# Kernel tuning notes

Measured on AMD Instinct MI355X. Metric: run time of the kernel, lower is better.

Reference implementation:

```python
import jax, jax.numpy as jnp
import numpy as np

WS = 2   # window_size
NH = 8   # num_heads


def window_attn(x, Wqkv, bqkv, scale, ws=WS, nh=NH):
    # x: (B, H, W, C) -> tiny ws*ws-token windowed MHA, faithful to torch reshape order
    B, H, W, C = x.shape
    hg, wg = H // ws, W // ws
    hd = C // nh
    xw = x.reshape(B, hg, ws, wg, ws, C).transpose(0, 1, 3, 2, 4, 5)  # (B,hg,wg,ws,ws,C)
    qkv = (xw @ Wqkv + bqkv).reshape(B, hg * wg, ws * ws, 3, nh, hd)
    q, k, v = jnp.transpose(qkv, (3, 0, 1, 4, 2, 5))  # each (B,G,nh,n,hd), n=ws*ws
    attn = jax.nn.softmax(jnp.einsum('bgnqd,bgnkd->bgnqk', q, k) * scale, axis=-1)
    o = jnp.einsum('bgnqk,bgnkd->bgnqd', attn, v)
    o = o.transpose(0, 1, 3, 2, 4).reshape(B, hg, wg, ws, ws, C)
    return o.transpose(0, 1, 3, 2, 4, 5).reshape(B, H, W, C)


def reference(x, Wqkv, bqkv, Wproj, bproj):
    B, C, H, W = x.shape
    scale = (C // NH) ** (-0.5)
    xr = x.reshape(B, H, W, C)  # raw reshape (NOT a transpose) -- faithful to source

    # --- Global path ---
    g = window_attn(xr, Wqkv, bqkv, scale) @ Wproj + bproj

    # --- Local path ---
    l = xr.reshape(B, C, H, W)                         # raw reshape, as in source
    l = l.reshape(B, C, H // 2, 2, W // 2, 2).mean(axis=(3, 5))  # AvgPool2d(2)
    h, w = H // 2, W // 2
    l = l.reshape(B, h, w, C)                          # raw reshape, as in source
    l = window_attn(l, Wqkv, bqkv, scale)
    l = l.reshape(B, C, h, w)                          # raw reshape, as in source
    # attn_x: reflect-pad top by 1, AvgPool2d((2,1), stride=1)
    px = jnp.pad(l, ((0, 0), (0, 0), (1, 0), (0, 0)), mode='reflect')
    lx = 0.5 * (px[:, :, :-1, :] + px[:, :, 1:, :])
    # attn_y: reflect-pad right by 1, AvgPool2d((1,2), stride=1)
    py = jnp.pad(l, ((0, 0), (0, 0), (0, 0), (0, 1)), mode='reflect')
    ly = 0.5 * (py[..., :-1] + py[..., 1:])
    # bilinear upsample x2, align_corners=False (half-pixel, matches jax.image.resize)
    l = jax.image.resize(lx + ly, (B, C, H, W), method='bilinear')
    l = l.reshape(B, H, W, C)                          # raw reshape, as in source

    return (g + l).transpose(0, 3, 1, 2)  # (B, C, H, W)


def setup_inputs() -> dict:
    key = jax.random.key(0)
    k1, k2, k3, k4, k5 = jax.random.split(key, 5)
    B, C, H, W = 4, 512, 128, 128
    x = jax.random.normal(k1, (B, C, H, W), dtype=jnp.float32)
    Wqkv = jax.random.normal(k2, (C, 3 * C), dtype=jnp.float32) * 0.02
    bqkv = jax.random.normal(k3, (3 * C,), dtype=jnp.float32) * 0.02
    Wproj = jax.random.normal(k4, (C, C), dtype=jnp.float32) * 0.02
    bproj = jax.random.normal(k5, (C,), dtype=jnp.float32) * 0.02
    return {'x': x, 'Wqkv': Wqkv, 'bqkv': bqkv, 'Wproj': Wproj, 'bproj': bproj}
```

## Files before the change

### kernel.cpp

```cpp
#include <hip/hip_runtime.h>

typedef float f32x4 __attribute__((ext_vector_type(4)));
typedef float f32x2 __attribute__((ext_vector_type(2)));
typedef __bf16 bf16x8 __attribute__((ext_vector_type(8)));
typedef __bf16 bf16x4 __attribute__((ext_vector_type(4)));

__device__ __forceinline__ void gll16(const void* g, void* l) {
  __builtin_amdgcn_global_load_lds(
      (const __attribute__((address_space(1))) uint32_t*)g,
      (__attribute__((address_space(3))) uint32_t*)l, 16, 0, 0);
}

__global__ __launch_bounds__(512, 2) void gemm256(
    const __bf16* __restrict__ A, const __bf16* __restrict__ BT,
    const float* __restrict__ bias, __bf16* __restrict__ C, int N, int gx)
{
  __shared__ __bf16 As[2][16384];
  __shared__ __bf16 Bs[2][16384];
  const int tid = threadIdx.x;
  const int wave = tid >> 6, lane = tid & 63;
  const int wr = (wave >> 2) * 128;
  const int wc = (wave & 3) * 64;
  const int l15 = lane & 15, l4 = lane >> 4;

  int lin = blockIdx.x;
  int olin = (lin & 7) * ((int)gridDim.x >> 3) + (lin >> 3);
  int bn = olin % gx, bm = olin / gx;
  const long arow0 = (long)bm * 256;
  const long brow0 = (long)bn * 256;

  const int srow = tid >> 3;
  const int sgc = ((tid & 7) ^ (srow & 7)) * 8;

  f32x4 acc[8][4] = {};

  auto stage = [&](int p, int kt) {
    #pragma unroll
    for (int s = 0; s < 4; s++) {
      int row = srow + s * 64;
      gll16(A  + (arow0 + row) * 512 + kt + sgc, (char*)As[p] + s * 8192 + tid * 16);
      gll16(BT + (brow0 + row) * 512 + kt + sgc, (char*)Bs[p] + s * 8192 + tid * 16);
    }
  };

  stage(0, 0);
  __syncthreads();

  for (int t = 0; t < 8; t++) {
    int cur = t & 1;
    if (t < 7) stage(cur ^ 1, (t + 1) * 64);
    #pragma unroll
    for (int kk = 0; kk < 2; kk++) {
      bf16x8 af[8], bfr[4];
      #pragma unroll
      for (int m = 0; m < 8; m++) {
        int row = wr + m * 16 + l15;
        int cp = ((kk * 4 + l4) ^ (row & 7)) * 8;
        af[m] = *(const bf16x8*)&As[cur][row * 64 + cp];
      }
      #pragma unroll
      for (int n = 0; n < 4; n++) {
        int row = wc + n * 16 + l15;
        int cp = ((kk * 4 + l4) ^ (row & 7)) * 8;
        bfr[n] = *(const bf16x8*)&Bs[cur][row * 64 + cp];
      }
      #pragma unroll
      for (int m = 0; m < 8; m++)
        #pragma unroll
        for (int n = 0; n < 4; n++)
          acc[m][n] = __builtin_amdgcn_mfma_f32_16x16x32_bf16(bfr[n], af[m], acc[m][n], 0, 0, 0);
    }
    if (t < 7) __syncthreads();
  }

  #pragma unroll
  for (int m = 0; m < 8; m++) {
    long row = arow0 + wr + m * 16 + l15;
    __bf16* crow = C + row * (long)N + brow0;
    #pragma unroll
    for (int n = 0; n < 4; n++) {
      f32x4 bv = *(const f32x4*)(bias + brow0 + wc + n * 16 + l4 * 4);
      bf16x4 o;
      #pragma unroll
      for (int k = 0; k < 4; k++) o[k] = (__bf16)(acc[m][n][k] + bv[k]);
      *(bf16x4*)(crow + wc + n * 16 + l4 * 4) = o;
    }
  }
}

__global__ __launch_bounds__(256) void attn4(
    const __bf16* __restrict__ qkv, __bf16* __restrict__ o,
    int nwin, int wg, int Wimg, int wpb, int bst)
{
  int tid = blockIdx.x * 256 + threadIdx.x;
  int m = tid & 3;
  int head = (tid >> 2) & 7;
  int win = tid >> 5;
  if (win >= nwin) return;
  int b = win / wpb, wrm = win % wpb;
  int i = wrm / wg, j = wrm % wg;
  int t0 = b * bst + 2 * i * Wimg + 2 * j;
  int tn[4] = { t0, t0 + 1, t0 + Wimg, t0 + Wimg + 1 };
  int trow = tn[m];
  const int co = head * 64;

  float qf[64];
  #pragma unroll
  for (int c = 0; c < 8; c++) {
    bf16x8 v = *(const bf16x8*)(qkv + (long)trow * 1536 + co + c * 8);
    #pragma unroll
    for (int e = 0; e < 8; e++) qf[c * 8 + e] = (float)v[e];
  }

  float s[4];
  #pragma unroll
  for (int n = 0; n < 4; n++) {
    float acc = 0.f;
    #pragma unroll
    for (int c = 0; c < 8; c++) {
      bf16x8 kv = *(const bf16x8*)(qkv + (long)tn[n] * 1536 + 512 + co + c * 8);
      #pragma unroll
      for (int e = 0; e < 8; e++) acc += qf[c * 8 + e] * (float)kv[e];
    }
    s[n] = acc * 0.125f;
  }

  float mx = fmaxf(fmaxf(s[0], s[1]), fmaxf(s[2], s[3]));
  float e0 = __expf(s[0] - mx), e1 = __expf(s[1] - mx),
        e2 = __expf(s[2] - mx), e3 = __expf(s[3] - mx);
  float inv = 1.f / (e0 + e1 + e2 + e3);
  float w4[4] = { e0 * inv, e1 * inv, e2 * inv, e3 * inv };

  float of[64] = {};
  #pragma unroll
  for (int n = 0; n < 4; n++) {
    float wn = w4[n];
    #pragma unroll
    for (int c = 0; c < 8; c++) {
      bf16x8 vv = *(const bf16x8*)(qkv + (long)tn[n] * 1536 + 1024 + co + c * 8);
      #pragma unroll
      for (int e = 0; e < 8; e++) of[c * 8 + e] += wn * (float)vv[e];
    }
  }

  #pragma unroll
  for (int c = 0; c < 8; c++) {
    bf16x8 ov;
    #pragma unroll
    for (int e = 0; e < 8; e++) ov[e] = (__bf16)of[c * 8 + e];
    *(bf16x8*)(o + (long)trow * 512 + co + c * 8) = ov;
  }
}

__global__ __launch_bounds__(256) void transpose_f32_bf16(
    const float* __restrict__ in, __bf16* __restrict__ out, int K, int N)
{
  __shared__ float t[64][65];
  int n0 = blockIdx.x * 64, k0 = blockIdx.y * 64;
  int tid = threadIdx.x;
  int nl4 = (tid & 15) * 4, kl = tid >> 4;
  #pragma unroll
  for (int p = 0; p < 4; p++) {
    int kk = kl + p * 16;
    f32x4 v = *(const f32x4*)(in + (long)(k0 + kk) * N + n0 + nl4);
    t[kk][nl4 + 0] = v.x; t[kk][nl4 + 1] = v.y; t[kk][nl4 + 2] = v.z; t[kk][nl4 + 3] = v.w;
  }
  __syncthreads();
  int ks = tid & 63, wv = tid >> 6;
  #pragma unroll
  for (int p = 0; p < 16; p++) {
    int nn = wv * 16 + p;
    out[(long)(n0 + nn) * K + k0 + ks] = (__bf16)t[ks][nn];
  }
}

__global__ __launch_bounds__(256) void convpool(const float* __restrict__ x,
    __bf16* __restrict__ Xbf, __bf16* __restrict__ P)
{
  int t = blockIdx.x * 256 + threadIdx.x;
  int j8 = (t & 15) * 8;
  int i2 = (t >> 4) & 63;
  long bc = t >> 10;
  const float* r0 = x + bc * 16384 + (2 * i2) * 128 + j8;
  f32x4 a0 = *(const f32x4*)r0,         a1 = *(const f32x4*)(r0 + 4);
  f32x4 b0 = *(const f32x4*)(r0 + 128), b1 = *(const f32x4*)(r0 + 132);
  bf16x8 xa, xb;
  xa[0] = (__bf16)a0.x; xa[1] = (__bf16)a0.y; xa[2] = (__bf16)a0.z; xa[3] = (__bf16)a0.w;
  xa[4] = (__bf16)a1.x; xa[5] = (__bf16)a1.y; xa[6] = (__bf16)a1.z; xa[7] = (__bf16)a1.w;
  xb[0] = (__bf16)b0.x; xb[1] = (__bf16)b0.y; xb[2] = (__bf16)b0.z; xb[3] = (__bf16)b0.w;
  xb[4] = (__bf16)b1.x; xb[5] = (__bf16)b1.y; xb[6] = (__bf16)b1.z; xb[7] = (__bf16)b1.w;
  *(bf16x8*)(Xbf + bc * 16384 + (2 * i2) * 128 + j8) = xa;
  *(bf16x8*)(Xbf + bc * 16384 + (2 * i2) * 128 + 128 + j8) = xb;
  bf16x4 p;
  p[0] = (__bf16)((a0.x + a0.y + b0.x + b0.y) * 0.25f);
  p[1] = (__bf16)((a0.z + a0.w + b0.z + b0.w) * 0.25f);
  p[2] = (__bf16)((a1.x + a1.y + b1.x + b1.y) * 0.25f);
  p[3] = (__bf16)((a1.z + a1.w + b1.z + b1.w) * 0.25f);
  *(bf16x4*)(P + bc * 4096 + i2 * 64 + (t & 15) * 4) = p;
}

__global__ __launch_bounds__(256) void final_v4(
    const __bf16* __restrict__ G, const __bf16* __restrict__ Ol, float* __restrict__ out)
{
  __shared__ float smem[12352];
  float (*t)[65] = (float(*)[65])smem;
  float* Sl = smem + 4160;
  __bf16* lbuf = (__bf16*)smem;

  int b = blockIdx.z;
  int p0 = blockIdx.y * 64, c0 = blockIdx.x * 64;
  int tid = threadIdx.x;

  {
    const __bf16* src = Ol + ((long)b * 512 + (long)blockIdx.y * 2) * 4096;
    #pragma unroll
    for (int i = 0; i < 4; i++)
      *(bf16x8*)&lbuf[i * 2048 + tid * 8] = *(const bf16x8*)(src + i * 2048 + tid * 8);
  }
  __syncthreads();

  #pragma unroll
  for (int k = 0; k < 32; k++) {
    int s = tid + k * 256;
    int j = s & 63, i = (s >> 6) & 63, lc = s >> 12;
    const __bf16* base = lbuf + lc * 4096;
    int im1 = (i == 0) ? 1 : i - 1;
    int jp1 = (j == 63) ? 62 : j + 1;
    Sl[s] = 0.5f * (float)base[im1 * 64 + j] + (float)base[i * 64 + j]
          + 0.5f * (float)base[i * 64 + jp1];
  }
  __syncthreads();

  int cl4 = (tid & 15) * 4, pl = tid >> 4;
  const __bf16* Gb = G + ((long)b * 16384 + p0) * 512 + c0;
  #pragma unroll
  for (int q2 = 0; q2 < 4; q2++) {
    int pp = pl + q2 * 16;
    bf16x4 g = *(const bf16x4*)(Gb + (long)pp * 512 + cl4);
    int q = (p0 + pp) * 512 + c0 + cl4;
    int lc = (q >> 14) & 1;
    int r = q & 16383, hh = r >> 7, ww0 = r & 127;
    const float* sb = Sl + lc * 4096;
    int i0, i1; float wi0, wi1;
    if (hh & 1) { i0 = hh >> 1; i1 = (i0 < 63) ? i0 + 1 : 63; wi0 = 0.75f; wi1 = 0.25f; }
    else        { i1 = hh >> 1; i0 = (i1 > 0) ? i1 - 1 : 0;   wi0 = 0.25f; wi1 = 0.75f; }
    int k = ww0 >> 1;
    int cm1 = (k > 0) ? k - 1 : 0;
    int cp2 = (k < 62) ? k + 2 : 63;
    const float* r0p = sb + i0 * 64;
    const float* r1p = sb + i1 * 64;
    float a0 = r0p[cm1], a1 = r0p[k], a2 = r0p[k + 1], a3 = r0p[cp2];
    float b0 = r1p[cm1], b1 = r1p[k], b2 = r1p[k + 1], b3 = r1p[cp2];
    float h0 = wi0 * (0.25f * a0 + 0.75f * a1) + wi1 * (0.25f * b0 + 0.75f * b1);
    float h1 = wi0 * (0.75f * a1 + 0.25f * a2) + wi1 * (0.75f * b1 + 0.25f * b2);
    float h2 = wi0 * (0.25f * a1 + 0.75f * a2) + wi1 * (0.25f * b1 + 0.75f * b2);
    float h3 = wi0 * (0.75f * a2 + 0.25f * a3) + wi1 * (0.75f * b2 + 0.25f * b3);
    t[pp][cl4 + 0] = (float)g[0] + h0;
    t[pp][cl4 + 1] = (float)g[1] + h1;
    t[pp][cl4 + 2] = (float)g[2] + h2;
    t[pp][cl4 + 3] = (float)g[3] + h3;
  }
  __syncthreads();
  int l15b = tid & 15, hi = (tid >> 4) & 3, wv = tid >> 6;
  float* ob = out + (long)b * 8388608 + (long)c0 * 16384 + p0;
  #pragma unroll
  for (int it = 0; it < 4; it++) {
    int cc = wv * 16 + it * 4 + hi;
    f32x4 v;
    v.x = t[l15b * 4 + 0][cc]; v.y = t[l15b * 4 + 1][cc];
    v.z = t[l15b * 4 + 2][cc]; v.w = t[l15b * 4 + 3][cc];
    *(f32x4*)(ob + (long)cc * 16384 + l15b * 4) = v;
  }
}

extern "C" void kernel_launch(void* const* d_in, const int* in_sizes, int n_in,
                              void* d_out, int out_size, void* d_ws, size_t ws_size,
                              hipStream_t stream)
{
  const float* x     = (const float*)d_in[0];
  const float* Wqkv  = (const float*)d_in[1];
  const float* bqkv  = (const float*)d_in[2];
  const float* Wproj = (const float*)d_in[3];
  const float* bproj = (const float*)d_in[4];
  float* out = (float*)d_out;

  char* w = (char*)d_ws;
  __bf16* WqkvT  = (__bf16*)w;  w += (size_t)1536 * 512 * 2;
  __bf16* WprojT = (__bf16*)w;  w += (size_t)512 * 512 * 2;
  __bf16* Xbf    = (__bf16*)w;  w += (size_t)65536 * 512 * 2;
  __bf16* G      = Xbf;
  __bf16* P      = (__bf16*)w;  w += (size_t)2048 * 4096 * 2;

  bool batched = ws_size >= ((size_t)356 << 20);
  size_t mchunk = batched ? 65536 : 16384;
  __bf16* QKVbuf = (__bf16*)w;  w += mchunk * 1536 * 2;
  __bf16* Obuf   = (__bf16*)w;

  transpose_f32_bf16<<<dim3(24, 8), 256, 0, stream>>>(Wqkv, WqkvT, 512, 1536);
  transpose_f32_bf16<<<dim3(8, 8), 256, 0, stream>>>(Wproj, WprojT, 512, 512);
  convpool<<<8192, 256, 0, stream>>>(x, Xbf, P);

  int nch = batched ? 1 : 4;
  int mrows = (int)mchunk;
  for (int c = 0; c < nch; c++) {
    const __bf16* Ac = Xbf + (size_t)c * 16384 * 512;
    gemm256<<<(mrows / 256) * 6, 512, 0, stream>>>(Ac, WqkvT, bqkv, QKVbuf, 1536, 6);
    attn4<<<(mrows / 4) * 32 / 256, 256, 0, stream>>>(
        QKVbuf, Obuf, mrows / 4, 64, 128, 4096, 16384);
    gemm256<<<(mrows / 256) * 2, 512, 0, stream>>>(
        Obuf, WprojT, bproj, G + (size_t)c * 16384 * 512, 512, 2);
  }

  gemm256<<<(16384 / 256) * 6, 512, 0, stream>>>(P, WqkvT, bqkv, QKVbuf, 1536, 6);
  attn4<<<512, 256, 0, stream>>>(QKVbuf, Obuf, 4096, 32, 64, 1024, 4096);

  final_v4<<<dim3(8, 256, 4), 256, 0, stream>>>(G, Obuf, out);
}
```

Before: 452.0 us.

## Split GEMM main loop into four phases interleaving chunked loads with MFMA

The GEMM k-loop is restructured into four sub-phases per k-tile. Each phase issues one quarter of the next tile's global-to-LDS loads, then computes one quadrant of the output tile, with explicit barriers, vmcnt waits and raised wave priority around the MFMAs. The goal is to spread load issue across the compute and hide memory latency better than staging the whole tile at once. The final epilogue kernel also remaps block indices so consecutive blocks touch different row regions, which may improve cache or channel locality. The extra barriers per tile add sync overhead, and the hand-written vmcnt counts must match the loads actually in flight.

```diff
diff --git a/kernel.cpp b/kernel.cpp
--- a/kernel.cpp
+++ b/kernel.cpp
@@ -11,7 +11,7 @@
       (__attribute__((address_space(3))) uint32_t*)l, 16, 0, 0);
 }
 
-__global__ __launch_bounds__(512, 2) void gemm256(
+__global__ __launch_bounds__(512, 2) void gemm256_8ph(
     const __bf16* __restrict__ A, const __bf16* __restrict__ BT,
     const float* __restrict__ bias, __bf16* __restrict__ C, int N, int gx)
 {
@@ -34,43 +34,65 @@
 
   f32x4 acc[8][4] = {};
 
-  auto stage = [&](int p, int kt) {
-    #pragma unroll
-    for (int s = 0; s < 4; s++) {
-      int row = srow + s * 64;
-      gll16(A  + (arow0 + row) * 512 + kt + sgc, (char*)As[p] + s * 8192 + tid * 16);
-      gll16(BT + (brow0 + row) * 512 + kt + sgc, (char*)Bs[p] + s * 8192 + tid * 16);
-    }
+  auto stage_chunk = [&](int p, int kt, int q) {
+    int row = srow + q * 64;
+    gll16(A  + (arow0 + row) * 512 + kt + sgc, (char*)As[p] + q * 8192 + tid * 16);
+    gll16(BT + (brow0 + row) * 512 + kt + sgc, (char*)Bs[p] + q * 8192 + tid * 16);
   };
 
-  stage(0, 0);
-  __syncthreads();
+  #pragma unroll
+  for (int q = 0; q < 4; q++) stage_chunk(0, 0, q);
 
   for (int t = 0; t < 8; t++) {
-    int cur = t & 1;
-    if (t < 7) stage(cur ^ 1, (t + 1) * 64);
-    #pragma unroll
-    for (int kk = 0; kk < 2; kk++) {
-      bf16x8 af[8], bfr[4];
+    int cur = t & 1, nxt = cur ^ 1;
+    __builtin_amdgcn_sched_barrier(0);
+    __builtin_amdgcn_s_barrier();
+    __builtin_amdgcn_sched_barrier(0);
+    if (t < 7) {
+      stage_chunk(nxt, (t + 1) * 64, 0);
+      asm volatile("s_waitcnt vmcnt(2)" ::: "memory");
+    } else {
+      asm volatile("s_waitcnt vmcnt(0)" ::: "memory");
+    }
+    __builtin_amdgcn_sched_barrier(0);
+    __builtin_amdgcn_s_barrier();
+    __builtin_amdgcn_sched_barrier(0);
+
+    #pragma unroll
+    for (int q = 0; q < 4; q++) {
+      if (q > 0) {
+        __builtin_amdgcn_sched_barrier(0);
+        __builtin_amdgcn_s_barrier();
+        __builtin_amdgcn_sched_barrier(0);
+        if (t < 7) stage_chunk(nxt, (t + 1) * 64, q);
+      }
+      const int mh = q >> 1, nh = q & 1;
       #pragma unroll
-      for (int m = 0; m < 8; m++) {
-        int row = wr + m * 16 + l15;
-        int cp = ((kk * 4 + l4) ^ (row & 7)) * 8;
-        af[m] = *(const bf16x8*)&As[cur][row * 64 + cp];
+      for (int kk = 0; kk < 2; kk++) {
+        bf16x8 af[4], bfr[2];
+        #pragma unroll
+        for (int i = 0; i < 4; i++) {
+          int row = wr + (mh * 4 + i) * 16 + l15;
+          int cp = (((kk * 4 + l4) ^ (row & 7))) * 8;
+          af[i] = *(const bf16x8*)&As[cur][row * 64 + cp];
+        }
+        #pragma unroll
+        for (int j = 0; j < 2; j++) {
+          int row = wc + (nh * 2 + j) * 16 + l15;
+          int cp = (((kk * 4 + l4) ^ (row & 7))) * 8;
+          bfr[j] = *(const bf16x8*)&Bs[cur][row * 64 + cp];
+        }
+        __builtin_amdgcn_s_setprio(1);
+        #pragma unroll
+        for (int i = 0; i < 4; i++)
+          #pragma unroll
+          for (int j = 0; j < 2; j++)
+            acc[mh * 4 + i][nh * 2 + j] =
+                __builtin_amdgcn_mfma_f32_16x16x32_bf16(bfr[j], af[i],
+                                                        acc[mh * 4 + i][nh * 2 + j], 0, 0, 0);
+        __builtin_amdgcn_s_setprio(0);
       }
-      #pragma unroll
-      for (int n = 0; n < 4; n++) {
-        int row = wc + n * 16 + l15;
-        int cp = ((kk * 4 + l4) ^ (row & 7)) * 8;
-        bfr[n] = *(const bf16x8*)&Bs[cur][row * 64 + cp];
-      }
-      #pragma unroll
-      for (int m = 0; m < 8; m++)
-        #pragma unroll
-        for (int n = 0; n < 4; n++)
-          acc[m][n] = __builtin_amdgcn_mfma_f32_16x16x32_bf16(bfr[n], af[m], acc[m][n], 0, 0, 0);
-    }
-    if (t < 7) __syncthreads();
+    }
   }
 
   #pragma unroll
@@ -199,7 +221,7 @@
   *(bf16x4*)(P + bc * 4096 + i2 * 64 + (t & 15) * 4) = p;
 }
 
-__global__ __launch_bounds__(256) void final_v4(
+__global__ __launch_bounds__(256) void final_v5(
     const __bf16* __restrict__ G, const __bf16* __restrict__ Ol, float* __restrict__ out)
 {
   __shared__ float smem[12352];
@@ -207,12 +229,16 @@
   float* Sl = smem + 4160;
   __bf16* lbuf = (__bf16*)smem;
 
+  int lin = blockIdx.x + (blockIdx.y << 3);
+  int r = lin & 7, k = lin >> 3;
+  int yy = r * 32 + (k >> 3);
+  int xx = k & 7;
   int b = blockIdx.z;
-  int p0 = blockIdx.y * 64, c0 = blockIdx.x * 64;
+  int p0 = yy * 64, c0 = xx * 64;
   int tid = threadIdx.x;
 
   {
-    const __bf16* src = Ol + ((long)b * 512 + (long)blockIdx.y * 2) * 4096;
+    const __bf16* src = Ol + ((long)b * 512 + (long)yy * 2) * 4096;
     #pragma unroll
     for (int i = 0; i < 4; i++)
       *(bf16x8*)&lbuf[i * 2048 + tid * 8] = *(const bf16x8*)(src + i * 2048 + tid * 8);
@@ -220,8 +246,8 @@
   __syncthreads();
 
   #pragma unroll
-  for (int k = 0; k < 32; k++) {
-    int s = tid + k * 256;
+  for (int kq = 0; kq < 32; kq++) {
+    int s = tid + kq * 256;
     int j = s & 63, i = (s >> 6) & 63, lc = s >> 12;
     const __bf16* base = lbuf + lc * 4096;
     int im1 = (i == 0) ? 1 : i - 1;
@@ -239,18 +265,18 @@
     bf16x4 g = *(const bf16x4*)(Gb + (long)pp * 512 + cl4);
     int q = (p0 + pp) * 512 + c0 + cl4;
     int lc = (q >> 14) & 1;
-    int r = q & 16383, hh = r >> 7, ww0 = r & 127;
+    int rr = q & 16383, hh = rr >> 7, ww0 = rr & 127;
     const float* sb = Sl + lc * 4096;
     int i0, i1; float wi0, wi1;
     if (hh & 1) { i0 = hh >> 1; i1 = (i0 < 63) ? i0 + 1 : 63; wi0 = 0.75f; wi1 = 0.25f; }
     else        { i1 = hh >> 1; i0 = (i1 > 0) ? i1 - 1 : 0;   wi0 = 0.25f; wi1 = 0.75f; }
-    int k = ww0 >> 1;
-    int cm1 = (k > 0) ? k - 1 : 0;
-    int cp2 = (k < 62) ? k + 2 : 63;
+    int kc = ww0 >> 1;
+    int cm1 = (kc > 0) ? kc - 1 : 0;
+    int cp2 = (kc < 62) ? kc + 2 : 63;
     const float* r0p = sb + i0 * 64;
     const float* r1p = sb + i1 * 64;
-    float a0 = r0p[cm1], a1 = r0p[k], a2 = r0p[k + 1], a3 = r0p[cp2];
-    float b0 = r1p[cm1], b1 = r1p[k], b2 = r1p[k + 1], b3 = r1p[cp2];
+    float a0 = r0p[cm1], a1 = r0p[kc], a2 = r0p[kc + 1], a3 = r0p[cp2];
+    float b0 = r1p[cm1], b1 = r1p[kc], b2 = r1p[kc + 1], b3 = r1p[cp2];
     float h0 = wi0 * (0.25f * a0 + 0.75f * a1) + wi1 * (0.25f * b0 + 0.75f * b1);
     float h1 = wi0 * (0.75f * a1 + 0.25f * a2) + wi1 * (0.75f * b1 + 0.25f * b2);
     float h2 = wi0 * (0.25f * a1 + 0.75f * a2) + wi1 * (0.25f * b1 + 0.75f * b2);
@@ -304,15 +330,15 @@
   int mrows = (int)mchunk;
   for (int c = 0; c < nch; c++) {
     const __bf16* Ac = Xbf + (size_t)c * 16384 * 512;
-    gemm256<<<(mrows / 256) * 6, 512, 0, stream>>>(Ac, WqkvT, bqkv, QKVbuf, 1536, 6);
+    gemm256_8ph<<<(mrows / 256) * 6, 512, 0, stream>>>(Ac, WqkvT, bqkv, QKVbuf, 1536, 6);
     attn4<<<(mrows / 4) * 32 / 256, 256, 0, stream>>>(
         QKVbuf, Obuf, mrows / 4, 64, 128, 4096, 16384);
-    gemm256<<<(mrows / 256) * 2, 512, 0, stream>>>(
+    gemm256_8ph<<<(mrows / 256) * 2, 512, 0, stream>>>(
         Obuf, WprojT, bproj, G + (size_t)c * 16384 * 512, 512, 2);
   }
 
-  gemm256<<<(16384 / 256) * 6, 512, 0, stream>>>(P, WqkvT, bqkv, QKVbuf, 1536, 6);
+  gemm256_8ph<<<(16384 / 256) * 6, 512, 0, stream>>>(P, WqkvT, bqkv, QKVbuf, 1536, 6);
   attn4<<<512, 256, 0, stream>>>(QKVbuf, Obuf, 4096, 32, 64, 1024, 4096);
 
-  final_v4<<<dim3(8, 256, 4), 256, 0, stream>>>(G, Obuf, out);
-}
+  final_v5<<<dim3(8, 256, 4), 256, 0, stream>>>(G, Obuf, out);
+}
```

Result: slower. 574.4 us (+27.1%).
